# Kernel tuning notes

Measured on AMD Instinct MI355X. Metric: run time of the kernel, lower is better.

## Reference

```python
import jax, jax.numpy as jnp
import numpy as np
import math

B, H, S, D = 256, 32, 16, 64
SCALE = 1.0 / math.sqrt(8.0)  # module hardcodes sqrt(8)
DROP_P = 0.3


def setup_inputs() -> dict:
    key = jax.random.key(0)
    kq, kk, kv = jax.random.split(key, 3)
    q = jax.random.normal(kq, (B, H, S, D), dtype=jnp.float32)
    k = jax.random.normal(kk, (B, H, S, D), dtype=jnp.float32)
    v = jax.random.normal(kv, (B, H, S, D), dtype=jnp.float32)
    return {"q": q, "k": k, "v": v}


def reference(q, k, v):
    # attn = (q @ k^T) / sqrt(8) + ones(16,16)
    attn = jnp.einsum("bhsd,bhtd->bhst", q, k) * SCALE
    attn = attn + jnp.ones((S, S), dtype=attn.dtype)  # additive mask (all ones)
    attn = jax.nn.softmax(attn, axis=-1)
    # dropout p=0.3 (training mode), fixed key for reproducibility
    keep = jax.random.bernoulli(jax.random.key(42), 1.0 - DROP_P, attn.shape)
    attn = jnp.where(keep, attn / (1.0 - DROP_P), 0.0)
    return jnp.einsum("bhst,bhtd->bhsd", attn, v)
```

## Files before the change

kernel.cpp:

```cpp
#include <hip/hip_runtime.h>
#include <stdint.h>
#include <stddef.h>


typedef __attribute__((ext_vector_type(8))) short short8;
typedef __attribute__((ext_vector_type(4))) float f32x4;

__device__ __forceinline__ unsigned short bf16_rne(float f) {
  unsigned u = __builtin_bit_cast(unsigned, f);
  unsigned r = 0x7FFFu + ((u >> 16) & 1u);
  return (unsigned short)((u + r) >> 16);
}
__device__ __forceinline__ float bf16_to_f32(unsigned short h) {
  unsigned u = ((unsigned)h) << 16;
  return __builtin_bit_cast(float, u);
}

__device__ __forceinline__ unsigned threefry_bits(unsigned idx) {
  const unsigned k0 = 0u, k1 = 42u;
  const unsigned k2 = k0 ^ k1 ^ 0x1BD11BDAu;
  unsigned x0 = k0;
  unsigned x1 = idx + k1;
#define TF_ROUND(r) { x0 += x1; x1 = (x1 << (r)) | (x1 >> (32 - (r))); x1 ^= x0; }
  TF_ROUND(13) TF_ROUND(15) TF_ROUND(26) TF_ROUND(6)
  x0 += k1; x1 += k2 + 1u;
  TF_ROUND(17) TF_ROUND(29) TF_ROUND(16) TF_ROUND(24)
  x0 += k2; x1 += k0 + 2u;
  TF_ROUND(13) TF_ROUND(15) TF_ROUND(26) TF_ROUND(6)
  x0 += k0; x1 += k1 + 3u;
  TF_ROUND(17) TF_ROUND(29) TF_ROUND(16) TF_ROUND(24)
  x0 += k1; x1 += k2 + 4u;
  TF_ROUND(13) TF_ROUND(15) TF_ROUND(26) TF_ROUND(6)
  x0 += k2; x1 += k0 + 5u;
#undef TF_ROUND
  return x0 ^ x1;
}

__device__ __forceinline__ void cvt_hilo_f4(float4 a, float4 b, short8& hi, short8& lo) {
  float x[8] = {a.x, a.y, a.z, a.w, b.x, b.y, b.z, b.w};
#pragma unroll
  for (int i = 0; i < 8; i++) {
    float f = x[i];
    unsigned short hs = bf16_rne(f);
    hi[i] = (short)hs;
    lo[i] = (short)bf16_rne(f - bf16_to_f32(hs));
  }
}

__global__ __launch_bounds__(256) void attn_kernel(
    const float* __restrict__ q, const float* __restrict__ k,
    const float* __restrict__ v, float* __restrict__ out) {
  __shared__ float vst[4][16 * 64];
  __shared__ float pst[4][16 * 20];

  const int lane = threadIdx.x & 63;
  const int w = threadIdx.x >> 6;
  const int bh = blockIdx.x * 4 + w;
  const int c = lane & 15;
  const int g = lane >> 4;

  const float* qp = q + (size_t)bh * 1024;
  const float* kp = k + (size_t)bh * 1024;
  const float* vp = v + (size_t)bh * 1024;
  float* op = out + (size_t)bh * 1024;

  const float4* qrow = (const float4*)(qp + c * 64 + g * 8);
  const float4* krow = (const float4*)(kp + c * 64 + g * 8);
  float4 qv0 = qrow[0], qv1 = qrow[1], qv2 = qrow[8], qv3 = qrow[9];
  float4 kv0 = krow[0], kv1 = krow[1], kv2 = krow[8], kv3 = krow[9];
  const float4* vsrc = (const float4*)vp;
  float4 vt0 = vsrc[lane], vt1 = vsrc[64 + lane], vt2 = vsrc[128 + lane], vt3 = vsrc[192 + lane];

  short8 qhi0, qlo0, qhi1, qlo1, khi0, klo0, khi1, klo1;
  cvt_hilo_f4(qv0, qv1, qhi0, qlo0);
  cvt_hilo_f4(qv2, qv3, qhi1, qlo1);
  cvt_hilo_f4(kv0, kv1, khi0, klo0);
  cvt_hilo_f4(kv2, kv3, khi1, klo1);

  f32x4 acc = {0.f, 0.f, 0.f, 0.f};
  acc = __builtin_amdgcn_mfma_f32_16x16x32_bf16(qhi0, khi0, acc, 0, 0, 0);
  acc = __builtin_amdgcn_mfma_f32_16x16x32_bf16(qhi1, khi1, acc, 0, 0, 0);
  acc = __builtin_amdgcn_mfma_f32_16x16x32_bf16(qlo0, khi0, acc, 0, 0, 0);
  acc = __builtin_amdgcn_mfma_f32_16x16x32_bf16(qlo1, khi1, acc, 0, 0, 0);
  acc = __builtin_amdgcn_mfma_f32_16x16x32_bf16(qhi0, klo0, acc, 0, 0, 0);
  acc = __builtin_amdgcn_mfma_f32_16x16x32_bf16(qhi1, klo1, acc, 0, 0, 0);

  const float SCALE = 0.35355339059327373f;
  float ad[4];
#pragma unroll
  for (int t = 0; t < 4; t++) {
    float sv = acc[t] * SCALE;
    float mx = sv;
#pragma unroll
    for (int msk = 1; msk < 16; msk <<= 1) mx = fmaxf(mx, __shfl_xor(mx, msk));
    float p = __expf(sv - mx);
    float sum = p;
#pragma unroll
    for (int msk = 1; msk < 16; msk <<= 1) sum += __shfl_xor(sum, msk);
    float aval = p / sum;
    unsigned idx = ((unsigned)bh << 8) + (unsigned)((4 * g + t) * 16 + c);
    unsigned bits = threefry_bits(idx);
    float u = __builtin_bit_cast(float, 0x3F800000u | (bits >> 9)) - 1.0f;
    ad[t] = (u < 0.7f) ? aval * (1.0f / 0.7f) : 0.0f;
  }

  float4* vw = (float4*)vst[w];
  vw[lane] = vt0; vw[64 + lane] = vt1; vw[128 + lane] = vt2; vw[192 + lane] = vt3;
  float* pb = pst[w];
#pragma unroll
  for (int t = 0; t < 4; t++) pb[(4 * g + t) * 20 + c] = ad[t];
  __syncthreads();

  short8 pa = {0, 0, 0, 0, 0, 0, 0, 0};
  if (g < 2) {
    const float* ps = pb + c * 20 + g * 8;
#pragma unroll
    for (int j = 0; j < 8; j++) pa[j] = (short)bf16_rne(ps[j]);
  }

  const float* vb_base = vst[w];
  f32x4 oacc[4];
#pragma unroll
  for (int nt = 0; nt < 4; nt++) {
    short8 vb = {0, 0, 0, 0, 0, 0, 0, 0};
    if (g < 2) {
#pragma unroll
      for (int j = 0; j < 8; j++)
        vb[j] = (short)bf16_rne(vb_base[(g * 8 + j) * 64 + nt * 16 + c]);
    }
    f32x4 z = {0.f, 0.f, 0.f, 0.f};
    oacc[nt] = __builtin_amdgcn_mfma_f32_16x16x32_bf16(pa, vb, z, 0, 0, 0);
  }

#pragma unroll
  for (int nt = 0; nt < 4; nt++)
#pragma unroll
    for (int t = 0; t < 4; t++)
      op[(4 * g + t) * 64 + nt * 16 + c] = oacc[nt][t];
}

extern "C" void kernel_launch(void* const* d_in, const int* in_sizes, int n_in,
                              void* d_out, int out_size, void* d_ws, size_t ws_size,
                              hipStream_t stream) {
  const float* q = (const float*)d_in[0];
  const float* k = (const float*)d_in[1];
  const float* v = (const float*)d_in[2];
  float* out = (float*)d_out;
  attn_kernel<<<2048, 256, 0, stream>>>(q, k, v, out);
}
```

Baseline: 133.1 us.

## Process two heads per wave with prefetched loads and bf16 LDS staging

Each wave now handles two (batch, head) slices and the grid is halved. All Q/K loads for both slices are issued up front, and the second V load is issued while the first slice is computed, so memory latency overlaps with compute. Both dropout masks are computed before the loop. The f32-to-bf16 split uses the packed bf16 conversion intrinsic. V and P are stored in LDS as bf16 with padded strides, and the block-wide __syncthreads is dropped in favour of wave-local LDS use. The cost is more registers per thread and half as many waves to hide latency, which may lower occupancy.

```diff
diff --git a/kernel.cpp b/kernel.cpp
--- a/kernel.cpp
+++ b/kernel.cpp
@@ -1,19 +1,28 @@
 #include <hip/hip_runtime.h>
+#include <hip/hip_bf16.h>
 #include <stdint.h>
 #include <stddef.h>
 
 
 typedef __attribute__((ext_vector_type(8))) short short8;
 typedef __attribute__((ext_vector_type(4))) float f32x4;
+typedef __attribute__((ext_vector_type(4))) unsigned int u32x4;
+
+#define VST 68
+#define PST 24
 
 __device__ __forceinline__ unsigned short bf16_rne(float f) {
   unsigned u = __builtin_bit_cast(unsigned, f);
   unsigned r = 0x7FFFu + ((u >> 16) & 1u);
   return (unsigned short)((u + r) >> 16);
 }
-__device__ __forceinline__ float bf16_to_f32(unsigned short h) {
-  unsigned u = ((unsigned)h) << 16;
-  return __builtin_bit_cast(float, u);
+
+__device__ __forceinline__ unsigned pk2_bf16(float a, float b) {
+  float2 t; t.x = a; t.y = b;
+  __hip_bfloat162 h = __float22bfloat162_rn(t);
+  unsigned r;
+  __builtin_memcpy(&r, &h, 4);
+  return r;
 }
 
 __device__ __forceinline__ unsigned threefry_bits(unsigned idx) {
@@ -36,107 +45,137 @@
   return x0 ^ x1;
 }
 
+__device__ __forceinline__ void drop_mask(int bh, int g, int c, float* m) {
+#pragma unroll
+  for (int t = 0; t < 4; t++) {
+    unsigned idx = ((unsigned)bh << 8) + (unsigned)((4 * g + t) * 16 + c);
+    unsigned bits = threefry_bits(idx);
+    float u = __builtin_bit_cast(float, 0x3F800000u | (bits >> 9)) - 1.0f;
+    m[t] = (u < 0.7f) ? (1.0f / 0.7f) : 0.0f;
+  }
+}
+
 __device__ __forceinline__ void cvt_hilo_f4(float4 a, float4 b, short8& hi, short8& lo) {
   float x[8] = {a.x, a.y, a.z, a.w, b.x, b.y, b.z, b.w};
+  u32x4 hw, lw;
 #pragma unroll
-  for (int i = 0; i < 8; i++) {
-    float f = x[i];
-    unsigned short hs = bf16_rne(f);
-    hi[i] = (short)hs;
-    lo[i] = (short)bf16_rne(f - bf16_to_f32(hs));
+  for (int i = 0; i < 4; i++) {
+    float e0 = x[2 * i], e1 = x[2 * i + 1];
+    unsigned hp = pk2_bf16(e0, e1);
+    float h0 = __builtin_bit_cast(float, hp << 16);
+    float h1 = __builtin_bit_cast(float, hp & 0xFFFF0000u);
+    unsigned lp = pk2_bf16(e0 - h0, e1 - h1);
+    hw[i] = hp; lw[i] = lp;
   }
+  hi = __builtin_bit_cast(short8, hw);
+  lo = __builtin_bit_cast(short8, lw);
 }
 
 __global__ __launch_bounds__(256) void attn_kernel(
     const float* __restrict__ q, const float* __restrict__ k,
     const float* __restrict__ v, float* __restrict__ out) {
-  __shared__ float vst[4][16 * 64];
-  __shared__ float pst[4][16 * 20];
+  __shared__ __align__(16) unsigned short vst[4][2][16 * VST];
+  __shared__ __align__(16) unsigned short pst[4][2][16 * PST];
 
   const int lane = threadIdx.x & 63;
   const int w = threadIdx.x >> 6;
-  const int bh = blockIdx.x * 4 + w;
+  const int wid = blockIdx.x * 4 + w;
   const int c = lane & 15;
   const int g = lane >> 4;
+  const int bh0 = wid, bh1 = wid + 4096;
 
-  const float* qp = q + (size_t)bh * 1024;
-  const float* kp = k + (size_t)bh * 1024;
-  const float* vp = v + (size_t)bh * 1024;
-  float* op = out + (size_t)bh * 1024;
+  float4 qv[2][4], kv[2][4], vt[2][4];
 
-  const float4* qrow = (const float4*)(qp + c * 64 + g * 8);
-  const float4* krow = (const float4*)(kp + c * 64 + g * 8);
-  float4 qv0 = qrow[0], qv1 = qrow[1], qv2 = qrow[8], qv3 = qrow[9];
-  float4 kv0 = krow[0], kv1 = krow[1], kv2 = krow[8], kv3 = krow[9];
-  const float4* vsrc = (const float4*)vp;
-  float4 vt0 = vsrc[lane], vt1 = vsrc[64 + lane], vt2 = vsrc[128 + lane], vt3 = vsrc[192 + lane];
+  const float4* qr0 = (const float4*)(q + (size_t)bh0 * 1024 + c * 64 + g * 8);
+  const float4* kr0 = (const float4*)(k + (size_t)bh0 * 1024 + c * 64 + g * 8);
+  qv[0][0] = qr0[0]; qv[0][1] = qr0[1]; qv[0][2] = qr0[8]; qv[0][3] = qr0[9];
+  kv[0][0] = kr0[0]; kv[0][1] = kr0[1]; kv[0][2] = kr0[8]; kv[0][3] = kr0[9];
+  const float4* vs0 = (const float4*)(v + (size_t)bh0 * 1024);
+#pragma unroll
+  for (int p2 = 0; p2 < 4; p2++) vt[0][p2] = vs0[p2 * 64 + lane];
 
-  short8 qhi0, qlo0, qhi1, qlo1, khi0, klo0, khi1, klo1;
-  cvt_hilo_f4(qv0, qv1, qhi0, qlo0);
-  cvt_hilo_f4(qv2, qv3, qhi1, qlo1);
-  cvt_hilo_f4(kv0, kv1, khi0, klo0);
-  cvt_hilo_f4(kv2, kv3, khi1, klo1);
+  const float4* qr1 = (const float4*)(q + (size_t)bh1 * 1024 + c * 64 + g * 8);
+  const float4* kr1 = (const float4*)(k + (size_t)bh1 * 1024 + c * 64 + g * 8);
+  qv[1][0] = qr1[0]; qv[1][1] = qr1[1]; qv[1][2] = qr1[8]; qv[1][3] = qr1[9];
+  kv[1][0] = kr1[0]; kv[1][1] = kr1[1]; kv[1][2] = kr1[8]; kv[1][3] = kr1[9];
 
-  f32x4 acc = {0.f, 0.f, 0.f, 0.f};
-  acc = __builtin_amdgcn_mfma_f32_16x16x32_bf16(qhi0, khi0, acc, 0, 0, 0);
-  acc = __builtin_amdgcn_mfma_f32_16x16x32_bf16(qhi1, khi1, acc, 0, 0, 0);
-  acc = __builtin_amdgcn_mfma_f32_16x16x32_bf16(qlo0, khi0, acc, 0, 0, 0);
-  acc = __builtin_amdgcn_mfma_f32_16x16x32_bf16(qlo1, khi1, acc, 0, 0, 0);
-  acc = __builtin_amdgcn_mfma_f32_16x16x32_bf16(qhi0, klo0, acc, 0, 0, 0);
-  acc = __builtin_amdgcn_mfma_f32_16x16x32_bf16(qhi1, klo1, acc, 0, 0, 0);
-
-  const float SCALE = 0.35355339059327373f;
-  float ad[4];
-#pragma unroll
-  for (int t = 0; t < 4; t++) {
-    float sv = acc[t] * SCALE;
-    float mx = sv;
-#pragma unroll
-    for (int msk = 1; msk < 16; msk <<= 1) mx = fmaxf(mx, __shfl_xor(mx, msk));
-    float p = __expf(sv - mx);
-    float sum = p;
-#pragma unroll
-    for (int msk = 1; msk < 16; msk <<= 1) sum += __shfl_xor(sum, msk);
-    float aval = p / sum;
-    unsigned idx = ((unsigned)bh << 8) + (unsigned)((4 * g + t) * 16 + c);
-    unsigned bits = threefry_bits(idx);
-    float u = __builtin_bit_cast(float, 0x3F800000u | (bits >> 9)) - 1.0f;
-    ad[t] = (u < 0.7f) ? aval * (1.0f / 0.7f) : 0.0f;
-  }
-
-  float4* vw = (float4*)vst[w];
-  vw[lane] = vt0; vw[64 + lane] = vt1; vw[128 + lane] = vt2; vw[192 + lane] = vt3;
-  float* pb = pst[w];
-#pragma unroll
-  for (int t = 0; t < 4; t++) pb[(4 * g + t) * 20 + c] = ad[t];
-  __syncthreads();
-
-  short8 pa = {0, 0, 0, 0, 0, 0, 0, 0};
-  if (g < 2) {
-    const float* ps = pb + c * 20 + g * 8;
-#pragma unroll
-    for (int j = 0; j < 8; j++) pa[j] = (short)bf16_rne(ps[j]);
-  }
-
-  const float* vb_base = vst[w];
-  f32x4 oacc[4];
-#pragma unroll
-  for (int nt = 0; nt < 4; nt++) {
-    short8 vb = {0, 0, 0, 0, 0, 0, 0, 0};
-    if (g < 2) {
-#pragma unroll
-      for (int j = 0; j < 8; j++)
-        vb[j] = (short)bf16_rne(vb_base[(g * 8 + j) * 64 + nt * 16 + c]);
-    }
-    f32x4 z = {0.f, 0.f, 0.f, 0.f};
-    oacc[nt] = __builtin_amdgcn_mfma_f32_16x16x32_bf16(pa, vb, z, 0, 0, 0);
-  }
+  float m[2][4];
+  drop_mask(bh0, g, c, m[0]);
+  drop_mask(bh1, g, c, m[1]);
 
 #pragma unroll
-  for (int nt = 0; nt < 4; nt++)
+  for (int it = 0; it < 2; it++) {
+    short8 qhi0, qlo0, qhi1, qlo1, khi0, klo0, khi1, klo1;
+    cvt_hilo_f4(qv[it][0], qv[it][1], qhi0, qlo0);
+    cvt_hilo_f4(qv[it][2], qv[it][3], qhi1, qlo1);
+    cvt_hilo_f4(kv[it][0], kv[it][1], khi0, klo0);
+    cvt_hilo_f4(kv[it][2], kv[it][3], khi1, klo1);
+
+    f32x4 acc = {0.f, 0.f, 0.f, 0.f};
+    acc = __builtin_amdgcn_mfma_f32_16x16x32_bf16(qhi0, khi0, acc, 0, 0, 0);
+    acc = __builtin_amdgcn_mfma_f32_16x16x32_bf16(qhi1, khi1, acc, 0, 0, 0);
+    acc = __builtin_amdgcn_mfma_f32_16x16x32_bf16(qlo0, khi0, acc, 0, 0, 0);
+    acc = __builtin_amdgcn_mfma_f32_16x16x32_bf16(qlo1, khi1, acc, 0, 0, 0);
+    acc = __builtin_amdgcn_mfma_f32_16x16x32_bf16(qhi0, klo0, acc, 0, 0, 0);
+    acc = __builtin_amdgcn_mfma_f32_16x16x32_bf16(qhi1, klo1, acc, 0, 0, 0);
+
+    const float SCALE = 0.35355339059327373f;
+    float ad[4];
 #pragma unroll
-    for (int t = 0; t < 4; t++)
-      op[(4 * g + t) * 64 + nt * 16 + c] = oacc[nt][t];
+    for (int t = 0; t < 4; t++) {
+      float sv = acc[t] * SCALE;
+      float mx = sv;
+#pragma unroll
+      for (int msk = 1; msk < 16; msk <<= 1) mx = fmaxf(mx, __shfl_xor(mx, msk));
+      float p = __expf(sv - mx);
+      float sum = p;
+#pragma unroll
+      for (int msk = 1; msk < 16; msk <<= 1) sum += __shfl_xor(sum, msk);
+      ad[t] = (p / sum) * m[it][t];
+    }
+
+    unsigned short* vw = &vst[w][it][0];
+#pragma unroll
+    for (int p2 = 0; p2 < 4; p2++) {
+      float4 vv = vt[it][p2];
+      unsigned w0 = pk2_bf16(vv.x, vv.y), w1 = pk2_bf16(vv.z, vv.w);
+      int t = 4 * p2 + g;
+      *(uint2*)(&vw[t * VST + 4 * c]) = make_uint2(w0, w1);
+    }
+
+    if (it == 0) {
+      const float4* vs1 = (const float4*)(v + (size_t)bh1 * 1024);
+#pragma unroll
+      for (int p2 = 0; p2 < 4; p2++) vt[1][p2] = vs1[p2 * 64 + lane];
+    }
+
+    unsigned short* pw = &pst[w][it][0];
+#pragma unroll
+    for (int t = 0; t < 4; t++) pw[(4 * g + t) * PST + c] = bf16_rne(ad[t]);
+
+    short8 pa = {0, 0, 0, 0, 0, 0, 0, 0};
+    if (g < 2) pa = *(const short8*)(&pw[c * PST + g * 8]);
+
+    f32x4 oacc[4];
+#pragma unroll
+    for (int nt = 0; nt < 4; nt++) {
+      short8 vb = {0, 0, 0, 0, 0, 0, 0, 0};
+      if (g < 2) {
+#pragma unroll
+        for (int j = 0; j < 8; j++)
+          vb[j] = (short)vw[(g * 8 + j) * VST + nt * 16 + c];
+      }
+      f32x4 z = {0.f, 0.f, 0.f, 0.f};
+      oacc[nt] = __builtin_amdgcn_mfma_f32_16x16x32_bf16(pa, vb, z, 0, 0, 0);
+    }
+
+    float* op = out + (size_t)(it == 0 ? bh0 : bh1) * 1024;
+#pragma unroll
+    for (int nt = 0; nt < 4; nt++)
+#pragma unroll
+      for (int t = 0; t < 4; t++)
+        op[(4 * g + t) * 64 + nt * 16 + c] = oacc[nt][t];
+  }
 }
 
 extern "C" void kernel_launch(void* const* d_in, const int* in_sizes, int n_in,
@@ -146,5 +185,5 @@
   const float* k = (const float*)d_in[1];
   const float* v = (const float*)d_in[2];
   float* out = (float*)d_out;
-  attn_kernel<<<2048, 256, 0, stream>>>(q, k, v, out);
+  attn_kernel<<<1024, 256, 0, stream>>>(q, k, v, out);
 }
```

Measured after the change: 133.8 us. Within noise of the previous version (+0.5%).
